# Kernel tuning notes

Measured on AMD Instinct MI355X. Metric: run time of the kernel, lower is better.

The kernel has to match this reference:

```python
import jax, jax.numpy as jnp
import numpy as np

B, S, D = 1, 4096, 2048
M = 4                  # compression rate
NC = S // M            # compressed slots
TOPK = 512
NH, C = 16, 64         # query heads, head dim
DC = 512               # query compression dim
NG, DG = 4, 512        # output projection groups, intermediate dim
CI, NHI = 64, 4        # indexer head dim, indexer heads
ROPE = 32              # partial rope dims (last ROPE of C)
EPS = 1e-6
NEG = -1e30


def _ln(x, w, b):
    mu = x.mean(-1, keepdims=True)
    var = ((x - mu) ** 2).mean(-1, keepdims=True)
    return (x - mu) * jax.lax.rsqrt(var + EPS) * w + b


def _rope(q, pos):
    # partial RoPE on the last ROPE dims of q [B,S,NH,C]; keys are NOT rotated (faithful)
    x_part, x_rope = q[..., :C - ROPE], q[..., C - ROPE:]
    x0, x1 = x_rope[..., 0::2], x_rope[..., 1::2]
    inv = 1.0 / (10000.0 ** (jnp.arange(0, ROPE, 2, dtype=jnp.float32) / ROPE))
    ang = pos[:, None].astype(jnp.float32) * inv[None]           # [S, ROPE/2]
    cos = jnp.cos(ang)[None, :, None, :]
    sin = jnp.sin(ang)[None, :, None, :]
    r = x0 * cos - x1 * sin
    i = x0 * sin + x1 * cos
    rot = jnp.stack([r, i], -1).reshape(x_rope.shape)
    return jnp.concatenate([x_part, rot], -1)


def reference(x, w_kv_a, w_kv_b, w_z_a, w_z_b, b_a, b_b, w_dq, w_iuq, w_w, w_k,
              w_uq, o_down, o_up, kvn_w, kvn_b, qn_w, qn_b, sink_logits):
    pos = jnp.arange(S)
    # ---- token-level compressor: windowed (2m-wide, m-stride) per-channel softmax ----
    c_a = (x @ w_kv_a).reshape(B, NC, M, C)
    c_b = (x @ w_kv_b).reshape(B, NC, M, C)
    z_a = (x @ w_z_a).reshape(B, NC, M, C)
    z_b = (x @ w_z_b).reshape(B, NC, M, C)
    prev_z = jnp.concatenate([jnp.full((B, 1, M, C), NEG, x.dtype), z_b[:, :-1]], 1)
    prev_c = jnp.concatenate([jnp.zeros((B, 1, M, C), x.dtype), c_b[:, :-1]], 1)
    logits = jnp.concatenate([prev_z + b_b, z_a + b_a], 2)        # [B,NC,2M,C]
    wts = jax.nn.softmax(logits, axis=2)
    compressed = (wts * jnp.concatenate([prev_c, c_a], 2)).sum(2)  # [B,NC,C]
    # ---- lightning indexer: relu multi-head scores + causal mask + top-k ----
    c_q = x @ w_dq                                                 # [B,S,DC]
    q_i = (c_q @ w_iuq).reshape(B, S, NHI, CI)
    hw = x @ w_w                                                   # [B,S,NHI]
    k_orig = x.reshape(B, NC, M, D).mean(2)
    k_proj = k_orig @ w_k                                          # [B,NC,CI]
    dot = jnp.einsum('bshc,bkc->bskh', q_i, k_proj)
    iscores = (jax.nn.relu(dot) * hw[:, :, None, :]).sum(-1)       # [B,S,NC]
    imask = jnp.arange(NC)[None, None, :] < pos[None, :, None]     # NC//S + 1 == 1
    iscores = jnp.where(imask, iscores, -jnp.inf)
    _, top_idx = jax.lax.top_k(iscores, TOPK)                      # [B,S,K]
    # ---- sparse attention over gathered compressed KV ----
    q = (c_q @ w_uq).reshape(B, S, NH, C)
    kc = _ln(compressed, kvn_w, kvn_b)
    q = _rope(_ln(q, qn_w, qn_b), pos)
    k_sel = kc[jnp.arange(B)[:, None, None], top_idx]              # [B,S,K,C]
    scores = jnp.einsum('bshc,bskc->bhsk', q, k_sel) / jnp.sqrt(jnp.float32(C))
    cmask = pos[None, None, :, None] < (top_idx[:, None, :, :] * M)
    scores = jnp.where(cmask, scores, -jnp.inf)
    e = jnp.exp(scores)
    denom = e.sum(-1, keepdims=True) + jnp.exp(sink_logits)[None, :, None, None]
    attn = e / denom                                               # sink-augmented softmax
    out = jnp.einsum('bhsk,bskc->bshc', attn, k_sel).reshape(B, S, NH * C)
    g = jnp.einsum('bsgd,gde->bsge', out.reshape(B, S, NG, (NH * C) // NG), o_down)
    return g.reshape(B, S, NG * DG) @ o_up


def setup_inputs() -> dict:
    key = jax.random.key(0)
    ks = jax.random.split(key, 20)
    lin = lambda k, fi, fo: jax.random.normal(k, (fi, fo), jnp.float32) / np.sqrt(fi)
    return {
        'x': jax.random.normal(ks[0], (B, S, D), jnp.float32),
        'w_kv_a': lin(ks[1], D, C), 'w_kv_b': lin(ks[2], D, C),
        'w_z_a': lin(ks[3], D, C), 'w_z_b': lin(ks[4], D, C),
        'b_a': 0.02 * jax.random.normal(ks[5], (M, C), jnp.float32),
        'b_b': 0.02 * jax.random.normal(ks[6], (M, C), jnp.float32),
        'w_dq': lin(ks[7], D, DC),
        'w_iuq': lin(ks[8], DC, CI * NHI),
        'w_w': lin(ks[9], D, NHI),
        'w_k': lin(ks[10], D, CI),
        'w_uq': lin(ks[11], DC, NH * C),
        'o_down': jax.random.normal(ks[12], (NG, (NH * C) // NG, DG), jnp.float32) / np.sqrt((NH * C) // NG),
        'o_up': lin(ks[13], NG * DG, D),
        'kvn_w': 1.0 + 0.02 * jax.random.normal(ks[14], (C,), jnp.float32),
        'kvn_b': 0.02 * jax.random.normal(ks[15], (C,), jnp.float32),
        'qn_w': 1.0 + 0.02 * jax.random.normal(ks[16], (C,), jnp.float32),
        'qn_b': 0.02 * jax.random.normal(ks[17], (C,), jnp.float32),
        'sink_logits': 0.02 * jax.random.normal(ks[18], (NH,), jnp.float32),
    }
```

## Files before the change

kernel.cpp:

```cpp
#include <hip/hip_runtime.h>
#include <math.h>

#define S_   4096
#define D_   2048
#define M_   4
#define NC_  1024
#define TOPK_ 512
#define NH_  16
#define C_   64
#define DC_  512
#define NG_  4
#define DG_  512
#define CI_  64
#define NHI_ 4
#define ROPE_ 32
#define EPS_ 1e-6f

typedef __attribute__((ext_vector_type(8))) short short8;
typedef __attribute__((ext_vector_type(4))) short short4v;
typedef __attribute__((ext_vector_type(4))) float floatx4;

__device__ inline unsigned short f2bf(float f) {
  unsigned u = __float_as_uint(f);
  u += 0x7fff + ((u >> 16) & 1);
  return (unsigned short)(u >> 16);
}
__device__ inline float bf2f(unsigned short h) {
  return __uint_as_float(((unsigned)h) << 16);
}

#define GLD16(src, dst) __builtin_amdgcn_global_load_lds( \
    (const __attribute__((address_space(1))) unsigned int*)(src), \
    (__attribute__((address_space(3))) unsigned int*)(dst), 16, 0, 0)

__device__ inline void xcd_remap(int& bx, int& by, int& bz) {
  int nx = gridDim.x, ny = gridDim.y;
  int flat = blockIdx.x + nx * (blockIdx.y + ny * blockIdx.z);
  int nwg = nx * ny * (int)gridDim.z;
  int swz = (flat & 7) * (nwg >> 3) + (flat >> 3);
  bx = swz % nx;
  int t = swz / nx;
  by = t % ny;
  bz = t / ny;
}

__global__ __launch_bounds__(256) void gemm_bf16_64(
    const unsigned short* __restrict__ A, const unsigned short* __restrict__ Bt,
    float* __restrict__ Cf, unsigned short* __restrict__ Cb,
    int K, int lda, int ldb, int ldc,
    long long Az, long long Bz, long long Cz) {
  int bx, by, zz;
  xcd_remap(bx, by, zz);
  A += (size_t)zz * Az;
  Bt += (size_t)zz * Bz;
  if (Cf) Cf += (size_t)zz * Cz;
  if (Cb) Cb += (size_t)zz * Cz;
  __shared__ unsigned short As[2 * 2 * 64 * 32];
  __shared__ unsigned short Bs[2 * 2 * 128 * 32];
  int tid = threadIdx.x;
  int bm = by * 64, bn = bx * 128;
  int lane = tid & 63, wid = tid >> 6;
  int wm = (wid & 1) * 32, wn = (wid >> 1) * 64;
  int qd = lane >> 4, m16 = lane & 15;

  floatx4 acc[2][4];
#pragma unroll
  for (int i = 0; i < 2; ++i)
#pragma unroll
    for (int j = 0; j < 4; ++j) acc[i][j] = (floatx4){0.f, 0.f, 0.f, 0.f};

  auto stage = [&](int buf, int kt) {
#pragma unroll
    for (int h = 0; h < 2; ++h) {
      {
        int rr = tid >> 2, ss = tid & 3;
        int gg = ss ^ ((rr >> 1) & 3);
        GLD16(A + (size_t)(bm + rr) * lda + kt + h * 32 + gg * 8,
              &As[(buf * 2 + h) * 2048 + tid * 8]);
      }
#pragma unroll
      for (int i = 0; i < 2; ++i) {
        int idx = tid + 256 * i;
        int rr = idx >> 2, ss = idx & 3;
        int gg = ss ^ ((rr >> 1) & 3);
        GLD16(Bt + (size_t)(bn + rr) * ldb + kt + h * 32 + gg * 8,
              &Bs[(buf * 2 + h) * 4096 + idx * 8]);
      }
    }
  };
  auto compute = [&](int buf) {
#pragma unroll
    for (int h = 0; h < 2; ++h) {
      const unsigned short* Ab = &As[(buf * 2 + h) * 2048];
      const unsigned short* Bb = &Bs[(buf * 2 + h) * 4096];
      short8 af[2], bfr[4];
#pragma unroll
      for (int mi = 0; mi < 2; ++mi) {
        int r = wm + mi * 16 + m16;
        int slot = qd ^ ((r >> 1) & 3);
        af[mi] = *(const short8*)&Ab[r * 32 + slot * 8];
      }
#pragma unroll
      for (int ni = 0; ni < 4; ++ni) {
        int r = wn + ni * 16 + m16;
        int slot = qd ^ ((r >> 1) & 3);
        bfr[ni] = *(const short8*)&Bb[r * 32 + slot * 8];
      }
#pragma unroll
      for (int mi = 0; mi < 2; ++mi)
#pragma unroll
        for (int ni = 0; ni < 4; ++ni)
          acc[mi][ni] = __builtin_amdgcn_mfma_f32_16x16x32_bf16(af[mi], bfr[ni], acc[mi][ni], 0, 0, 0);
    }
  };

  stage(0, 0);
  __syncthreads();
  int cur = 0;
  for (int kt = 64; kt < K; kt += 64) {
    stage(cur ^ 1, kt);
    compute(cur);
    __syncthreads();
    cur ^= 1;
  }
  compute(cur);

#pragma unroll
  for (int mi = 0; mi < 2; ++mi)
#pragma unroll
    for (int ni = 0; ni < 4; ++ni) {
      int col = bn + wn + ni * 16 + m16;
#pragma unroll
      for (int rg = 0; rg < 4; ++rg) {
        int row = bm + wm + mi * 16 + qd * 4 + rg;
        if (Cb)
          Cb[(size_t)row * ldc + col] = f2bf(acc[mi][ni][rg]);
        else
          Cf[(size_t)row * ldc + col] = acc[mi][ni][rg];
      }
    }
}

__global__ __launch_bounds__(256) void gemm_bf16_128(
    const unsigned short* __restrict__ A, const unsigned short* __restrict__ Bt,
    float* __restrict__ Cf, unsigned short* __restrict__ Cb,
    int K, int lda, int ldb, int ldc,
    long long Az, long long Bz, long long Cz) {
  int bx, by, zz;
  xcd_remap(bx, by, zz);
  A += (size_t)zz * Az;
  Bt += (size_t)zz * Bz;
  if (Cf) Cf += (size_t)zz * Cz;
  if (Cb) Cb += (size_t)zz * Cz;
  __shared__ unsigned short As[2 * 2 * 128 * 32];
  __shared__ unsigned short Bs[2 * 2 * 128 * 32];
  int tid = threadIdx.x;
  int bm = by * 128, bn = bx * 128;
  int lane = tid & 63, wid = tid >> 6;
  int wm = (wid & 1) * 64, wn = (wid >> 1) * 64;
  int qd = lane >> 4, m16 = lane & 15;

  floatx4 acc[4][4];
#pragma unroll
  for (int i = 0; i < 4; ++i)
#pragma unroll
    for (int j = 0; j < 4; ++j) acc[i][j] = (floatx4){0.f, 0.f, 0.f, 0.f};

  auto stage = [&](int buf, int kt) {
#pragma unroll
    for (int h = 0; h < 2; ++h) {
#pragma unroll
      for (int i = 0; i < 2; ++i) {
        int idx = tid + 256 * i;
        int rr = idx >> 2, ss = idx & 3;
        int gg = ss ^ ((rr >> 1) & 3);
        GLD16(A + (size_t)(bm + rr) * lda + kt + h * 32 + gg * 8,
              &As[(buf * 2 + h) * 4096 + idx * 8]);
        GLD16(Bt + (size_t)(bn + rr) * ldb + kt + h * 32 + gg * 8,
              &Bs[(buf * 2 + h) * 4096 + idx * 8]);
      }
    }
  };
  auto compute = [&](int buf) {
#pragma unroll
    for (int h = 0; h < 2; ++h) {
      const unsigned short* Ab = &As[(buf * 2 + h) * 4096];
      const unsigned short* Bb = &Bs[(buf * 2 + h) * 4096];
      short8 af[4], bfr[4];
#pragma unroll
      for (int mi = 0; mi < 4; ++mi) {
        int r = wm + mi * 16 + m16;
        int slot = qd ^ ((r >> 1) & 3);
        af[mi] = *(const short8*)&Ab[r * 32 + slot * 8];
      }
#pragma unroll
      for (int ni = 0; ni < 4; ++ni) {
        int r = wn + ni * 16 + m16;
        int slot = qd ^ ((r >> 1) & 3);
        bfr[ni] = *(const short8*)&Bb[r * 32 + slot * 8];
      }
#pragma unroll
      for (int mi = 0; mi < 4; ++mi)
#pragma unroll
        for (int ni = 0; ni < 4; ++ni)
          acc[mi][ni] = __builtin_amdgcn_mfma_f32_16x16x32_bf16(af[mi], bfr[ni], acc[mi][ni], 0, 0, 0);
    }
  };

  stage(0, 0);
  __syncthreads();
  int cur = 0;
  for (int kt = 64; kt < K; kt += 64) {
    stage(cur ^ 1, kt);
    compute(cur);
    __syncthreads();
    cur ^= 1;
  }
  compute(cur);

#pragma unroll
  for (int mi = 0; mi < 4; ++mi)
#pragma unroll
    for (int ni = 0; ni < 4; ++ni) {
      int col = bn + wn + ni * 16 + m16;
#pragma unroll
      for (int rg = 0; rg < 4; ++rg) {
        int row = bm + wm + mi * 16 + qd * 4 + rg;
        if (Cb)
          Cb[(size_t)row * ldc + col] = f2bf(acc[mi][ni][rg]);
        else
          Cf[(size_t)row * ldc + col] = acc[mi][ni][rg];
      }
    }
}

__global__ __launch_bounds__(256) void gemm_bf16_split_64(
    const unsigned short* __restrict__ Ah, const unsigned short* __restrict__ Al,
    const unsigned short* __restrict__ Bh, const unsigned short* __restrict__ Bl,
    float* __restrict__ Cf, int K, int lda, int ldb, int ldc,
    long long Az, long long Bz, long long Cz) {
  int bx, by, zz;
  xcd_remap(bx, by, zz);
  Ah += (size_t)zz * Az; Al += (size_t)zz * Az;
  Bh += (size_t)zz * Bz; Bl += (size_t)zz * Bz;
  Cf += (size_t)zz * Cz;
  __shared__ unsigned short Ash[64 * 32];
  __shared__ unsigned short Asl[64 * 32];
  __shared__ unsigned short Bsh[128 * 32];
  __shared__ unsigned short Bsl[128 * 32];
  int tid = threadIdx.x;
  int bm = by * 64, bn = bx * 128;
  int lane = tid & 63, wid = tid >> 6;
  int wm = (wid & 1) * 32, wn = (wid >> 1) * 64;
  int qd = lane >> 4, m16 = lane & 15;

  floatx4 acc[2][4];
#pragma unroll
  for (int i = 0; i < 2; ++i)
#pragma unroll
    for (int j = 0; j < 4; ++j) acc[i][j] = (floatx4){0.f, 0.f, 0.f, 0.f};

  for (int k0 = 0; k0 < K; k0 += 32) {
    {
      int r = tid >> 2, sl = tid & 3;
      int g = sl ^ ((r >> 1) & 3);
      size_t aoff = (size_t)(bm + r) * lda + k0 + g * 8;
      GLD16(Ah + aoff, &Ash[tid * 8]);
      GLD16(Al + aoff, &Asl[tid * 8]);
    }
#pragma unroll
    for (int i = 0; i < 2; ++i) {
      int idx = tid + 256 * i;
      int r = idx >> 2, sl = idx & 3;
      int g = sl ^ ((r >> 1) & 3);
      size_t boff = (size_t)(bn + r) * ldb + k0 + g * 8;
      GLD16(Bh + boff, &Bsh[idx * 8]);
      GLD16(Bl + boff, &Bsl[idx * 8]);
    }
    __syncthreads();
    short8 afh[2], afl[2], bfh[4], bfl[4];
#pragma unroll
    for (int mi = 0; mi < 2; ++mi) {
      int r = wm + mi * 16 + m16;
      int slot = qd ^ ((r >> 1) & 3);
      afh[mi] = *(const short8*)&Ash[r * 32 + slot * 8];
      afl[mi] = *(const short8*)&Asl[r * 32 + slot * 8];
    }
#pragma unroll
    for (int ni = 0; ni < 4; ++ni) {
      int r = wn + ni * 16 + m16;
      int slot = qd ^ ((r >> 1) & 3);
      bfh[ni] = *(const short8*)&Bsh[r * 32 + slot * 8];
      bfl[ni] = *(const short8*)&Bsl[r * 32 + slot * 8];
    }
#pragma unroll
    for (int mi = 0; mi < 2; ++mi)
#pragma unroll
      for (int ni = 0; ni < 4; ++ni) {
        acc[mi][ni] = __builtin_amdgcn_mfma_f32_16x16x32_bf16(afh[mi], bfh[ni], acc[mi][ni], 0, 0, 0);
        acc[mi][ni] = __builtin_amdgcn_mfma_f32_16x16x32_bf16(afh[mi], bfl[ni], acc[mi][ni], 0, 0, 0);
        acc[mi][ni] = __builtin_amdgcn_mfma_f32_16x16x32_bf16(afl[mi], bfh[ni], acc[mi][ni], 0, 0, 0);
      }
    __syncthreads();
  }
#pragma unroll
  for (int mi = 0; mi < 2; ++mi)
#pragma unroll
    for (int ni = 0; ni < 4; ++ni) {
      int col = bn + wn + ni * 16 + m16;
#pragma unroll
      for (int rg = 0; rg < 4; ++rg) {
        int row = bm + wm + mi * 16 + qd * 4 + rg;
        Cf[(size_t)row * ldc + col] = acc[mi][ni][rg];
      }
    }
}

__global__ __launch_bounds__(256) void gemm_bf16_split_128(
    const unsigned short* __restrict__ Ah, const unsigned short* __restrict__ Al,
    const unsigned short* __restrict__ Bh, const unsigned short* __restrict__ Bl,
    float* __restrict__ Cf, int K, int lda, int ldb, int ldc,
    long long Az, long long Bz, long long Cz) {
  int bx, by, zz;
  xcd_remap(bx, by, zz);
  Ah += (size_t)zz * Az; Al += (size_t)zz * Az;
  Bh += (size_t)zz * Bz; Bl += (size_t)zz * Bz;
  Cf += (size_t)zz * Cz;
  __shared__ unsigned short Ash[2 * 128 * 32];
  __shared__ unsigned short Asl[2 * 128 * 32];
  __shared__ unsigned short Bsh[2 * 128 * 32];
  __shared__ unsigned short Bsl[2 * 128 * 32];
  int tid = threadIdx.x;
  int bm = by * 128, bn = bx * 128;
  int lane = tid & 63, wid = tid >> 6;
  int wm = (wid & 1) * 64, wn = (wid >> 1) * 64;
  int qd = lane >> 4, m16 = lane & 15;

  floatx4 acc[4][4];
#pragma unroll
  for (int i = 0; i < 4; ++i)
#pragma unroll
    for (int j = 0; j < 4; ++j) acc[i][j] = (floatx4){0.f, 0.f, 0.f, 0.f};

  auto stage = [&](int buf, int kt) {
#pragma unroll
    for (int i = 0; i < 2; ++i) {
      int idx = tid + 256 * i;
      int rr = idx >> 2, ss = idx & 3;
      int gg = ss ^ ((rr >> 1) & 3);
      size_t aoff = (size_t)(bm + rr) * lda + kt + gg * 8;
      size_t boff = (size_t)(bn + rr) * ldb + kt + gg * 8;
      GLD16(Ah + aoff, &Ash[buf * 4096 + idx * 8]);
      GLD16(Al + aoff, &Asl[buf * 4096 + idx * 8]);
      GLD16(Bh + boff, &Bsh[buf * 4096 + idx * 8]);
      GLD16(Bl + boff, &Bsl[buf * 4096 + idx * 8]);
    }
  };
  auto compute = [&](int buf) {
    const unsigned short* Ahb = &Ash[buf * 4096];
    const unsigned short* Alb = &Asl[buf * 4096];
    const unsigned short* Bhb = &Bsh[buf * 4096];
    const unsigned short* Blb = &Bsl[buf * 4096];
    short8 afh[4], afl[4], bfh[4], bfl[4];
#pragma unroll
    for (int mi = 0; mi < 4; ++mi) {
      int r = wm + mi * 16 + m16;
      int slot = qd ^ ((r >> 1) & 3);
      afh[mi] = *(const short8*)&Ahb[r * 32 + slot * 8];
      afl[mi] = *(const short8*)&Alb[r * 32 + slot * 8];
    }
#pragma unroll
    for (int ni = 0; ni < 4; ++ni) {
      int r = wn + ni * 16 + m16;
      int slot = qd ^ ((r >> 1) & 3);
      bfh[ni] = *(const short8*)&Bhb[r * 32 + slot * 8];
      bfl[ni] = *(const short8*)&Blb[r * 32 + slot * 8];
    }
#pragma unroll
    for (int mi = 0; mi < 4; ++mi)
#pragma unroll
      for (int ni = 0; ni < 4; ++ni) {
        acc[mi][ni] = __builtin_amdgcn_mfma_f32_16x16x32_bf16(afh[mi], bfh[ni], acc[mi][ni], 0, 0, 0);
        acc[mi][ni] = __builtin_amdgcn_mfma_f32_16x16x32_bf16(afh[mi], bfl[ni], acc[mi][ni], 0, 0, 0);
        acc[mi][ni] = __builtin_amdgcn_mfma_f32_16x16x32_bf16(afl[mi], bfh[ni], acc[mi][ni], 0, 0, 0);
      }
  };

  stage(0, 0);
  __syncthreads();
  int cur = 0;
  for (int kt = 32; kt < K; kt += 32) {
    stage(cur ^ 1, kt);
    compute(cur);
    __syncthreads();
    cur ^= 1;
  }
  compute(cur);

#pragma unroll
  for (int mi = 0; mi < 4; ++mi)
#pragma unroll
    for (int ni = 0; ni < 4; ++ni) {
      int col = bn + wn + ni * 16 + m16;
#pragma unroll
      for (int rg = 0; rg < 4; ++rg) {
        int row = bm + wm + mi * 16 + qd * 4 + rg;
        Cf[(size_t)row * ldc + col] = acc[mi][ni][rg];
      }
    }
}

__global__ void reduce_f32(const float* __restrict__ P, float* __restrict__ C, int n, int z) {
  int i = (blockIdx.x * 256 + threadIdx.x) * 4;
  if (i >= n) return;
  float4 a = *(const float4*)&P[i];
  for (int s = 1; s < z; ++s) {
    float4 b = *(const float4*)&P[(size_t)s * n + i];
    a.x += b.x; a.y += b.y; a.z += b.z; a.w += b.w;
  }
  *(float4*)&C[i] = a;
}

__global__ void reduce_cast_split(const float* __restrict__ P, unsigned short* __restrict__ hi,
                                  unsigned short* __restrict__ lo, int n, int z) {
  int i = (blockIdx.x * 256 + threadIdx.x) * 4;
  if (i >= n) return;
  float4 a = *(const float4*)&P[i];
  for (int s = 1; s < z; ++s) {
    float4 b = *(const float4*)&P[(size_t)s * n + i];
    a.x += b.x; a.y += b.y; a.z += b.z; a.w += b.w;
  }
  ushort4 h = make_ushort4(f2bf(a.x), f2bf(a.y), f2bf(a.z), f2bf(a.w));
  ushort4 l = make_ushort4(f2bf(a.x - bf2f(h.x)), f2bf(a.y - bf2f(h.y)),
                           f2bf(a.z - bf2f(h.z)), f2bf(a.w - bf2f(h.w)));
  *(ushort4*)&hi[i] = h;
  *(ushort4*)&lo[i] = l;
}

__global__ __launch_bounds__(256) void iscores_mfma(
    const unsigned short* __restrict__ Ah, const unsigned short* __restrict__ Al,
    const unsigned short* __restrict__ Bh, const unsigned short* __restrict__ Bl,
    const float* __restrict__ hw, float* __restrict__ isc) {
  int bm = blockIdx.y * 128, bn = blockIdx.x * 128;
  if (bn > (bm >> 2) + 30) return;
  __shared__ unsigned short Ash[128 * 32];
  __shared__ unsigned short Asl[128 * 32];
  __shared__ unsigned short Bsh[128 * 32];
  __shared__ unsigned short Bsl[128 * 32];
  int tid = threadIdx.x;
  int lane = tid & 63, wid = tid >> 6;
  int wm = (wid >> 1) * 64, wn = (wid & 1) * 64;
  int qd = lane >> 4, m16 = lane & 15;

  floatx4 acc[4][4];
#pragma unroll
  for (int i = 0; i < 4; ++i)
#pragma unroll
    for (int j = 0; j < 4; ++j) acc[i][j] = (floatx4){0.f, 0.f, 0.f, 0.f};

#pragma unroll
  for (int k0 = 0; k0 < 64; k0 += 32) {
#pragma unroll
    for (int i = 0; i < 2; ++i) {
      int idx = tid + 256 * i;
      int r = idx >> 2, s = idx & 3;
      int g = s ^ ((r >> 1) & 3);
      size_t aoff = (size_t)(bm + r) * 64 + k0 + g * 8;
      size_t boff = (size_t)(bn + r) * 64 + k0 + g * 8;
      GLD16(Ah + aoff, &Ash[idx * 8]);
      GLD16(Al + aoff, &Asl[idx * 8]);
      GLD16(Bh + boff, &Bsh[idx * 8]);
      GLD16(Bl + boff, &Bsl[idx * 8]);
    }
    __syncthreads();
    short8 afh[4], afl[4], bfh[4], bfl[4];
#pragma unroll
    for (int mi = 0; mi < 4; ++mi) {
      int r = wm + mi * 16 + m16;
      int slot = qd ^ ((r >> 1) & 3);
      afh[mi] = *(const short8*)&Ash[r * 32 + slot * 8];
      afl[mi] = *(const short8*)&Asl[r * 32 + slot * 8];
    }
#pragma unroll
    for (int ni = 0; ni < 4; ++ni) {
      int r = wn + ni * 16 + m16;
      int slot = qd ^ ((r >> 1) & 3);
      bfh[ni] = *(const short8*)&Bsh[r * 32 + slot * 8];
      bfl[ni] = *(const short8*)&Bsl[r * 32 + slot * 8];
    }
#pragma unroll
    for (int mi = 0; mi < 4; ++mi)
#pragma unroll
      for (int ni = 0; ni < 4; ++ni) {
        acc[mi][ni] = __builtin_amdgcn_mfma_f32_16x16x32_bf16(afh[mi], bfh[ni], acc[mi][ni], 0, 0, 0);
        acc[mi][ni] = __builtin_amdgcn_mfma_f32_16x16x32_bf16(afh[mi], bfl[ni], acc[mi][ni], 0, 0, 0);
        acc[mi][ni] = __builtin_amdgcn_mfma_f32_16x16x32_bf16(afl[mi], bfh[ni], acc[mi][ni], 0, 0, 0);
      }
    __syncthreads();
  }
#pragma unroll
  for (int mi = 0; mi < 4; ++mi) {
    int tok = ((bm + wm + mi * 16) >> 2) + qd;
    float4 hwv = *(const float4*)&hw[tok * 4];
#pragma unroll
    for (int ni = 0; ni < 4; ++ni) {
      floatx4 a = acc[mi][ni];
      float v = fmaxf(a[0], 0.f) * hwv.x + fmaxf(a[1], 0.f) * hwv.y +
                fmaxf(a[2], 0.f) * hwv.z + fmaxf(a[3], 0.f) * hwv.w;
      int col = bn + wn + ni * 16 + m16;
      isc[(size_t)tok * NC_ + col] = (col < tok) ? v : -__builtin_inff();
    }
  }
}

#define BM 64
#define BN 64
#define BK 16
#define KSL_ 16
#define KSLICE_ 128
__global__ __launch_bounds__(256) void gemm_f32_splitk(
    const float* __restrict__ A, const float* __restrict__ B,
    float* __restrict__ P, int lda, int ldb) {
  __shared__ float As[BK][BM + 4];
  __shared__ float Bs[BK][BN + 4];
  int tid = threadIdx.x;
  int bm = blockIdx.y * BM;
  int kbase = blockIdx.x * KSLICE_;
  int tr = tid >> 4;
  int tc = tid & 15;
  float acc[4][4] = {{0.f}};
  for (int k0 = kbase; k0 < kbase + KSLICE_; k0 += BK) {
    int ac = tid & 15;
    int ar0 = tid >> 4;
#pragma unroll
    for (int i = 0; i < 4; ++i) {
      int r = ar0 + 16 * i;
      As[ac][r] = A[(size_t)(bm + r) * lda + k0 + ac];
    }
    int bc = tid & 63;
    int br0 = tid >> 6;
#pragma unroll
    for (int i = 0; i < 4; ++i) {
      int r = br0 + 4 * i;
      Bs[r][bc] = B[(size_t)(k0 + r) * ldb + bc];
    }
    __syncthreads();
#pragma unroll
    for (int kk = 0; kk < BK; ++kk) {
      float4 av = *(const float4*)&As[kk][tr * 4];
      float4 bv = *(const float4*)&Bs[kk][tc * 4];
      float a[4] = {av.x, av.y, av.z, av.w};
      float b[4] = {bv.x, bv.y, bv.z, bv.w};
#pragma unroll
      for (int i = 0; i < 4; ++i)
#pragma unroll
        for (int j = 0; j < 4; ++j) acc[i][j] += a[i] * b[j];
    }
    __syncthreads();
  }
  float* Pb = P + (size_t)blockIdx.x * (NC_ * CI_);
#pragma unroll
  for (int i = 0; i < 4; ++i) {
    float4 v = make_float4(acc[i][0], acc[i][1], acc[i][2], acc[i][3]);
    *(float4*)&Pb[(size_t)(bm + tr * 4 + i) * CI_ + tc * 4] = v;
  }
}

__global__ void reduce_splitk_cast(const float* __restrict__ P,
                                   unsigned short* __restrict__ hi,
                                   unsigned short* __restrict__ lo) {
  int i = blockIdx.x * 256 + threadIdx.x;
  float a = 0.f;
#pragma unroll
  for (int s = 0; s < KSL_; ++s) a += P[(size_t)s * (NC_ * CI_) + i];
  unsigned short h = f2bf(a);
  hi[i] = h;
  lo[i] = f2bf(a - bf2f(h));
}

__device__ inline float wave_sum64(float v) {
#pragma unroll
  for (int off = 32; off > 0; off >>= 1) v += __shfl_xor(v, off, 64);
  return v;
}

__global__ __launch_bounds__(512) void cast_split_hw_mean(
    const float* __restrict__ x, unsigned short* __restrict__ hi,
    unsigned short* __restrict__ lo, const float* __restrict__ ww,
    float* __restrict__ hw, float* __restrict__ ko) {
  int j = blockIdx.x, tid = threadIdx.x;
  int d0 = tid * 4;
  const float* wr = ww + d0 * 4;
  float4 v[4];
  float a[4][4];
#pragma unroll
  for (int m = 0; m < 4; ++m) {
    size_t i = (size_t)(j * 4 + m) * D_ + d0;
    v[m] = *(const float4*)&x[i];
    ushort4 h = make_ushort4(f2bf(v[m].x), f2bf(v[m].y), f2bf(v[m].z), f2bf(v[m].w));
    ushort4 l = make_ushort4(f2bf(v[m].x - bf2f(h.x)), f2bf(v[m].y - bf2f(h.y)),
                             f2bf(v[m].z - bf2f(h.z)), f2bf(v[m].w - bf2f(h.w)));
    *(ushort4*)&hi[i] = h;
    *(ushort4*)&lo[i] = l;
    a[m][0] = v[m].x * wr[0] + v[m].y * wr[4] + v[m].z * wr[8]  + v[m].w * wr[12];
    a[m][1] = v[m].x * wr[1] + v[m].y * wr[5] + v[m].z * wr[9]  + v[m].w * wr[13];
    a[m][2] = v[m].x * wr[2] + v[m].y * wr[6] + v[m].z * wr[10] + v[m].w * wr[14];
    a[m][3] = v[m].x * wr[3] + v[m].y * wr[7] + v[m].z * wr[11] + v[m].w * wr[15];
  }
  float4 s4;
  s4.x = 0.25f * (v[0].x + v[1].x + v[2].x + v[3].x);
  s4.y = 0.25f * (v[0].y + v[1].y + v[2].y + v[3].y);
  s4.z = 0.25f * (v[0].z + v[1].z + v[2].z + v[3].z);
  s4.w = 0.25f * (v[0].w + v[1].w + v[2].w + v[3].w);
  *(float4*)&ko[(size_t)j * D_ + d0] = s4;
#pragma unroll
  for (int m = 0; m < 4; ++m)
#pragma unroll
    for (int h2 = 0; h2 < 4; ++h2) a[m][h2] = wave_sum64(a[m][h2]);
  __shared__ float red[8][16];
  int wid = tid >> 6, lane = tid & 63;
  if (lane == 0) {
#pragma unroll
    for (int m = 0; m < 4; ++m)
#pragma unroll
      for (int h2 = 0; h2 < 4; ++h2) red[wid][m * 4 + h2] = a[m][h2];
  }
  __syncthreads();
  if (tid < 16) {
    float acc = 0.f;
#pragma unroll
    for (int w2 = 0; w2 < 8; ++w2) acc += red[w2][tid];
    hw[(size_t)(j * 4 + (tid >> 2)) * 4 + (tid & 3)] = acc;
  }
}

__global__ __launch_bounds__(256) void prep_kernel(
    const float* __restrict__ w_kv_a, const float* __restrict__ w_kv_b,
    const float* __restrict__ w_z_a, const float* __restrict__ w_z_b,
    unsigned short* __restrict__ wpackT,
    const float* __restrict__ w_dq, unsigned short* __restrict__ wdqTh,
    unsigned short* __restrict__ wdqTl,
    const float* __restrict__ w_iuq, unsigned short* __restrict__ wiuqTh,
    unsigned short* __restrict__ wiuqTl,
    const float* __restrict__ w_uq, unsigned short* __restrict__ wuqT,
    const float* __restrict__ o_down, unsigned short* __restrict__ odb,
    const float* __restrict__ o_up, unsigned short* __restrict__ oupT,
    float* __restrict__ rt) {
  __shared__ float t[32][33];
  int b = blockIdx.x;
  int tid = threadIdx.x;
  int tx = tid & 31, ty = tid >> 5;
  if (b < 512) {
    int wsel = b >> 7, local = b & 127;
    int bx = local & 63, by = local >> 6;
    const float* in = (wsel == 0) ? w_kv_a : (wsel == 1) ? w_kv_b : (wsel == 2) ? w_z_a : w_z_b;
    unsigned short* outp = wpackT + wsel * 64 * 2048;
    int k0 = bx * 32, n0 = by * 32;
#pragma unroll
    for (int i = 0; i < 4; ++i)
      t[ty * 4 + i][tx] = in[(size_t)(k0 + ty * 4 + i) * 64 + n0 + tx];
    __syncthreads();
#pragma unroll
    for (int i = 0; i < 4; ++i)
      outp[(size_t)(n0 + ty * 4 + i) * 2048 + k0 + tx] = f2bf(t[tx][ty * 4 + i]);
  } else if (b < 1536) {
    int local = b - 512;
    int bx = local & 63, by = local >> 6;
    int k0 = bx * 32, n0 = by * 32;
#pragma unroll
    for (int i = 0; i < 4; ++i)
      t[ty * 4 + i][tx] = w_dq[(size_t)(k0 + ty * 4 + i) * 512 + n0 + tx];
    __syncthreads();
#pragma unroll
    for (int i = 0; i < 4; ++i) {
      float v = t[tx][ty * 4 + i];
      unsigned short h = f2bf(v);
      wdqTh[(size_t)(n0 + ty * 4 + i) * 2048 + k0 + tx] = h;
      wdqTl[(size_t)(n0 + ty * 4 + i) * 2048 + k0 + tx] = f2bf(v - bf2f(h));
    }
  } else if (b < 1664) {
    int local = b - 1536;
    int bx = local & 15, by = local >> 4;
    int k0 = bx * 32, n0 = by * 32;
#pragma unroll
    for (int i = 0; i < 4; ++i)
      t[ty * 4 + i][tx] = w_iuq[(size_t)(k0 + ty * 4 + i) * 256 + n0 + tx];
    __syncthreads();
#pragma unroll
    for (int i = 0; i < 4; ++i) {
      float v = t[tx][ty * 4 + i];
      unsigned short h = f2bf(v);
      wiuqTh[(size_t)(n0 + ty * 4 + i) * 512 + k0 + tx] = h;
      wiuqTl[(size_t)(n0 + ty * 4 + i) * 512 + k0 + tx] = f2bf(v - bf2f(h));
    }
  } else if (b < 2176) {
    int local = b - 1664;
    int bx = local & 15, by = local >> 4;
    int k0 = bx * 32, n0 = by * 32;
#pragma unroll
    for (int i = 0; i < 4; ++i)
      t[ty * 4 + i][tx] = w_uq[(size_t)(k0 + ty * 4 + i) * 1024 + n0 + tx];
    __syncthreads();
#pragma unroll
    for (int i = 0; i < 4; ++i)
      wuqT[(size_t)(n0 + ty * 4 + i) * 512 + k0 + tx] = f2bf(t[tx][ty * 4 + i]);
  } else if (b < 2688) {
    int i = ((b - 2176) * 256 + tid) * 4;
    float4 v = *(const float4*)&o_down[i];
    ushort4 o = make_ushort4(f2bf(v.x), f2bf(v.y), f2bf(v.z), f2bf(v.w));
    *(ushort4*)&odb[i] = o;
  } else if (b < 6784) {
    int local = b - 2688;
    int bx = local & 63, by = local >> 6;
    int k0 = bx * 32, n0 = by * 32;
#pragma unroll
    for (int i = 0; i < 4; ++i)
      t[ty * 4 + i][tx] = o_up[(size_t)(k0 + ty * 4 + i) * 2048 + n0 + tx];
    __syncthreads();
#pragma unroll
    for (int i = 0; i < 4; ++i)
      oupT[(size_t)(n0 + ty * 4 + i) * 2048 + k0 + tx] = f2bf(t[tx][ty * 4 + i]);
  } else {
    int i = (b - 6784) * 256 + tid;
    int s = i >> 4, p = i & 15;
    float inv = powf(10000.f, -(2.f * (float)p) / (float)ROPE_);
    float ang = (float)s * inv;
    rt[i * 2] = cosf(ang);
    rt[i * 2 + 1] = sinf(ang);
  }
}

__global__ void gate_ln_kernel(const float* __restrict__ c4,
                               const float* __restrict__ ba, const float* __restrict__ bb,
                               const float* __restrict__ w, const float* __restrict__ bias,
                               unsigned short* __restrict__ kcb,
                               unsigned short* __restrict__ kcbT) {
  int i = blockIdx.x * 256 + threadIdx.x;
  int j = i >> 6, c = i & 63;
  float lg[8], vv[8];
#pragma unroll
  for (int m = 0; m < 4; ++m) {
    if (j == 0) {
      lg[m] = -1e30f + bb[m * C_ + c];
      vv[m] = 0.f;
    } else {
      int row = (j - 1) * 4 + m;
      lg[m] = c4[(size_t)row * 256 + 192 + c] + bb[m * C_ + c];
      vv[m] = c4[(size_t)row * 256 + 64 + c];
    }
    int row2 = j * 4 + m;
    lg[4 + m] = c4[(size_t)row2 * 256 + 128 + c] + ba[m * C_ + c];
    vv[4 + m] = c4[(size_t)row2 * 256 + 0 + c];
  }
  float mx = lg[0];
#pragma unroll
  for (int t = 1; t < 8; ++t) mx = fmaxf(mx, lg[t]);
  float se = 0.f, acc = 0.f;
#pragma unroll
  for (int t = 0; t < 8; ++t) {
    float e = expf(lg[t] - mx);
    se += e;
    acc += e * vv[t];
  }
  float cv = acc / se;
  float mu = wave_sum64(cv) * (1.f / 64.f);
  float d = cv - mu;
  float var = wave_sum64(d * d) * (1.f / 64.f);
  float y = d * (1.f / sqrtf(var + EPS_)) * w[c] + bias[c];
  unsigned short h = f2bf(y);
  kcb[(size_t)j * C_ + c] = h;
  kcbT[(size_t)c * NC_ + j] = h;
}

__global__ void ln_rope_q_kernel(const float* __restrict__ quq, const float* __restrict__ w,
                                 const float* __restrict__ b, const float* __restrict__ rt,
                                 unsigned short* __restrict__ qb) {
  int row = blockIdx.x * 4 + (threadIdx.x >> 6);
  int s = row >> 4;
  int c = threadIdx.x & 63;
  float v = quq[(size_t)row * C_ + c];
  float mu = wave_sum64(v) * (1.f / 64.f);
  float d = v - mu;
  float var = wave_sum64(d * d) * (1.f / 64.f);
  float y = d * (1.f / sqrtf(var + EPS_)) * w[c] + b[c];
  float outv;
  float partner = __shfl_xor(y, 1, 64);
  if (c < C_ - ROPE_) {
    outv = y;
  } else {
    int p = (c - (C_ - ROPE_)) >> 1;
    float cs = rt[(s * 16 + p) * 2];
    float sn = rt[(s * 16 + p) * 2 + 1];
    if ((c & 1) == 0)
      outv = y * cs - partner * sn;
    else
      outv = partner * sn + y * cs;
  }
  qb[(size_t)row * C_ + c] = f2bf(outv * 0.125f);
}

#define MINF_ 0x007FFFFFu
__global__ __launch_bounds__(256) void topk_select_kernel(
    const float* __restrict__ isc, unsigned* __restrict__ sel) {
  __shared__ unsigned mv[NC_];
  __shared__ unsigned bins[256];
  __shared__ unsigned wsum[4];
  __shared__ unsigned sB, sR;
  __shared__ unsigned selw[32];
  int s = blockIdx.x;
  int tid = threadIdx.x;
  int w = tid >> 6, lane = tid & 63;
  if (tid < 32) selw[tid] = 0u;
  for (int i = tid; i < NC_; i += 256) {
    if (i < s) {
      unsigned u = __float_as_uint(isc[(size_t)s * NC_ + i]);
      mv[i] = (u & 0x80000000u) ? ~u : (u | 0x80000000u);
    } else {
      mv[i] = MINF_;
    }
  }
  __syncthreads();
  unsigned K_rem = TOPK_;
  unsigned prefix = 0u;
  for (int lvl = 0; lvl < 4; ++lvl) {
    int shift = 24 - 8 * lvl;
    unsigned pm = (lvl == 0) ? 0u : (0xFFFFFFFFu << (32 - 8 * lvl));
    bins[tid] = 0u;
    __syncthreads();
    for (int i = tid; i < NC_; i += 256) {
      unsigned m = mv[i];
      if ((m & pm) == prefix) atomicAdd(&bins[(m >> shift) & 0xFFu], 1u);
    }
    __syncthreads();
    unsigned v = bins[tid];
    unsigned p = v;
#pragma unroll
    for (int off = 1; off < 64; off <<= 1) {
      unsigned n = __shfl_up(p, (unsigned)off, 64);
      if (lane >= off) p += n;
    }
    if (lane == 63) wsum[w] = p;
    __syncthreads();
    unsigned T = 0, woff = 0;
#pragma unroll
    for (int i = 0; i < 4; ++i) {
      unsigned x_ = wsum[i];
      T += x_;
      if (i < w) woff += x_;
    }
    p += woff;
    unsigned gt = T - p;
    if (gt < K_rem && K_rem <= gt + v) { sB = (unsigned)tid; sR = K_rem - gt; }
    __syncthreads();
    prefix |= (sB << shift);
    K_rem = sR;
  }
  unsigned vstar = prefix;
  unsigned eq = 0;
#pragma unroll
  for (int j = 0; j < 4; ++j) eq += (mv[4 * tid + j] == vstar);
  unsigned rp = eq;
#pragma unroll
  for (int off = 1; off < 64; off <<= 1) {
    unsigned n = __shfl_up(rp, (unsigned)off, 64);
    if (lane >= off) rp += n;
  }
  if (lane == 63) wsum[w] = rp;
  __syncthreads();
  unsigned woff2 = 0;
#pragma unroll
  for (int i = 0; i < 4; ++i)
    if (i < w) woff2 += wsum[i];
  unsigned rank0 = rp + woff2 - eq;
  unsigned local = 0, bits = 0;
#pragma unroll
  for (int j = 0; j < 4; ++j) {
    unsigned m = mv[4 * tid + j];
    int idx = 4 * tid + j;
    bool sb = ((m > vstar) || (m == vstar && (rank0 + local) < K_rem)) && (s < 4 * idx);
    local += (m == vstar);
    if (sb) bits |= (1u << (idx & 31));
  }
  if (bits) atomicOr(&selw[tid >> 3], bits);
  __syncthreads();
  if (tid < 32) sel[(size_t)s * 32 + tid] = selw[tid];
}

#define TS_ 8
__global__ __launch_bounds__(256) void attn_mfma_kernel(
    const unsigned short* __restrict__ qb, const unsigned short* __restrict__ kcb,
    const unsigned short* __restrict__ kcbT, const unsigned* __restrict__ sel,
    const float* __restrict__ sink, unsigned short* __restrict__ out) {
  __shared__ unsigned short p_s[128 * 68];
  __shared__ unsigned selw[TS_][32];
  int tid = threadIdx.x;
  int s0 = blockIdx.x * TS_;
  int lane = tid & 63, w = tid >> 6;
  int qd = lane >> 4, m16 = lane & 15;

  selw[tid >> 5][tid & 31] = sel[(size_t)(s0 + (tid >> 5)) * 32 + (tid & 31)];

  short8 qf[2][2];
#pragma unroll
  for (int tk = 0; tk < 2; ++tk)
#pragma unroll
    for (int ks = 0; ks < 2; ++ks)
      qf[tk][ks] = *(const short8*)&qb[(size_t)(s0 + 2 * w + tk) * 1024 + m16 * 64 + ks * 32 + qd * 8];

  floatx4 of[2][4];
#pragma unroll
  for (int i = 0; i < 2; ++i)
#pragma unroll
    for (int j = 0; j < 4; ++j) of[i][j] = (floatx4){0.f, 0.f, 0.f, 0.f};
  float dsum[2] = {0.f, 0.f};

  int ub = max(511, s0 + TS_ - 2);
  int ct_start = max(0, (s0 + 4) >> 8);
  int ct_end = min(16, (ub >> 6) + 1);

  for (int ct = ct_start; ct < ct_end; ++ct) {
    int c0 = ct * 64;
#pragma unroll
    for (int mc = 0; mc < 4; ++mc) {
      short8 a0 = *(const short8*)&kcb[(size_t)(c0 + mc * 16 + m16) * 64 + qd * 8];
      short8 a1 = *(const short8*)&kcb[(size_t)(c0 + mc * 16 + m16) * 64 + 32 + qd * 8];
#pragma unroll
      for (int nt = 0; nt < 2; ++nt) {
        floatx4 sc = (floatx4){0.f, 0.f, 0.f, 0.f};
        sc = __builtin_amdgcn_mfma_f32_16x16x32_bf16(a0, qf[nt][0], sc, 0, 0, 0);
        sc = __builtin_amdgcn_mfma_f32_16x16x32_bf16(a1, qf[nt][1], sc, 0, 0, 0);
        int tokL = 2 * w + nt;
        unsigned sw = selw[tokL][ct * 2 + (mc >> 1)];
        short4v pv;
#pragma unroll
        for (int rg = 0; rg < 4; ++rg) {
          int bitpos = (mc * 16 + qd * 4 + rg) & 31;
          bool ok = ((sw >> bitpos) & 1u) != 0u;
          float e = ok ? __expf(sc[rg]) : 0.f;
          dsum[nt] += e;
          pv[rg] = (short)f2bf(e);
        }
        *(short4v*)&p_s[(tokL * 16 + m16) * 68 + mc * 16 + qd * 4] = pv;
      }
    }
#pragma unroll
    for (int ks = 0; ks < 2; ++ks) {
      short8 pa0 = *(const short8*)&p_s[((2 * w + 0) * 16 + m16) * 68 + ks * 32 + qd * 8];
      short8 pa1 = *(const short8*)&p_s[((2 * w + 1) * 16 + m16) * 68 + ks * 32 + qd * 8];
#pragma unroll
      for (int nt = 0; nt < 4; ++nt) {
        short8 bv = *(const short8*)&kcbT[(size_t)(nt * 16 + m16) * NC_ + c0 + ks * 32 + qd * 8];
        of[0][nt] = __builtin_amdgcn_mfma_f32_16x16x32_bf16(pa0, bv, of[0][nt], 0, 0, 0);
        of[1][nt] = __builtin_amdgcn_mfma_f32_16x16x32_bf16(pa1, bv, of[1][nt], 0, 0, 0);
      }
    }
  }
#pragma unroll
  for (int nt = 0; nt < 2; ++nt) {
    dsum[nt] += __shfl_xor(dsum[nt], 16, 64);
    dsum[nt] += __shfl_xor(dsum[nt], 32, 64);
  }
#pragma unroll
  for (int tk = 0; tk < 2; ++tk)
#pragma unroll
    for (int nt = 0; nt < 4; ++nt) {
      floatx4 o = of[tk][nt];
#pragma unroll
      for (int rg = 0; rg < 4; ++rg) {
        int head = qd * 4 + rg;
        float dn = __shfl(dsum[tk], head, 64) + __expf(sink[head]);
        out[(size_t)(s0 + 2 * w + tk) * 1024 + head * 64 + nt * 16 + m16] = f2bf(o[rg] / dn);
      }
    }
}

#define OFF_QUQ    0u
#define OFF_Q      4194304u
#define OFF_XH     8388608u
#define OFF_XL     12582912u
#define OFF_PART   16777216u
#define OFF_KO     18874368u
#define OFF_C4     20971520u
#define OFF_CQF    22020096u
#define OFF_RT     23134208u
#define OFF_WTB    24117248u
#define OFF_CQH    25165824u
#define OFF_CQL    26214400u
#define OFF_WPACKT 27262976u
#define OFF_WDQTH  27525120u
#define OFF_WDQTL  28049408u
#define OFF_WIUQTH 28573696u
#define OFF_WIUQTL 28639232u
#define OFF_WUQT   28704768u
#define OFF_ODB    28966912u
#define OFF_OUPT   29229056u
#define OFF_HW     31326208u
#define OFF_KC     31408128u
#define OFF_KPR    31473664u

extern "C" void kernel_launch(void* const* d_in, const int* in_sizes, int n_in,
                              void* d_out, int out_size, void* d_ws, size_t ws_size,
                              hipStream_t stream) {
  const float* x      = (const float*)d_in[0];
  const float* w_kv_a = (const float*)d_in[1];
  const float* w_kv_b = (const float*)d_in[2];
  const float* w_z_a  = (const float*)d_in[3];
  const float* w_z_b  = (const float*)d_in[4];
  const float* b_a    = (const float*)d_in[5];
  const float* b_b    = (const float*)d_in[6];
  const float* w_dq   = (const float*)d_in[7];
  const float* w_iuq  = (const float*)d_in[8];
  const float* w_w    = (const float*)d_in[9];
  const float* w_k    = (const float*)d_in[10];
  const float* w_uq   = (const float*)d_in[11];
  const float* o_down = (const float*)d_in[12];
  const float* o_up   = (const float*)d_in[13];
  const float* kvn_w  = (const float*)d_in[14];
  const float* kvn_b  = (const float*)d_in[15];
  const float* qn_w   = (const float*)d_in[16];
  const float* qn_b   = (const float*)d_in[17];
  const float* sink   = (const float*)d_in[18];
  float* out = (float*)d_out;
  float* ws = (float*)d_ws;

  float* quq   = ws + OFF_QUQ;
  float* isc   = ws + OFF_QUQ;
  unsigned short* qb = (unsigned short*)(ws + OFF_Q);
  unsigned short* xh = (unsigned short*)(ws + OFF_XH);
  unsigned short* xl = (unsigned short*)(ws + OFF_XL);
  unsigned* sel = (unsigned*)(ws + OFF_XL);
  float* part  = ws + OFF_PART;
  float* k_or  = ws + OFF_KO;
  unsigned short* attnb = (unsigned short*)(ws + OFF_KO);
  float* c4    = ws + OFF_C4;
  unsigned short* qih = (unsigned short*)(ws + OFF_CQF);
  unsigned short* qil = qih + S_ * NHI_ * CI_;
  unsigned short* kph = qil + S_ * NHI_ * CI_;
  unsigned short* kpl = kph + NC_ * CI_;
  float* rt    = ws + OFF_RT;
  unsigned short* wtb = (unsigned short*)(ws + OFF_WTB);
  unsigned short* cqh = (unsigned short*)(ws + OFF_CQH);
  unsigned short* cql = (unsigned short*)(ws + OFF_CQL);
  unsigned short* wpackT = (unsigned short*)(ws + OFF_WPACKT);
  unsigned short* wdqTh  = (unsigned short*)(ws + OFF_WDQTH);
  unsigned short* wdqTl  = (unsigned short*)(ws + OFF_WDQTL);
  unsigned short* wiuqTh = (unsigned short*)(ws + OFF_WIUQTH);
  unsigned short* wiuqTl = (unsigned short*)(ws + OFF_WIUQTL);
  unsigned short* wuqT   = (unsigned short*)(ws + OFF_WUQT);
  unsigned short* odb    = (unsigned short*)(ws + OFF_ODB);
  unsigned short* oupT   = (unsigned short*)(ws + OFF_OUPT);
  float* hw    = ws + OFF_HW;
  unsigned short* kcb  = (unsigned short*)(ws + OFF_KC);
  unsigned short* kcbT = kcb + NC_ * C_;

  dim3 blk(256);

  cast_split_hw_mean<<<NC_, dim3(512), 0, stream>>>(x, xh, xl, w_w, hw, k_or);
  prep_kernel<<<7040, blk, 0, stream>>>(w_kv_a, w_kv_b, w_z_a, w_z_b, wpackT,
                                        w_dq, wdqTh, wdqTl, w_iuq, wiuqTh, wiuqTl,
                                        w_uq, wuqT, o_down, odb, o_up, oupT, rt);

  gemm_bf16_64<<<dim3(2, 32, 4), blk, 0, stream>>>(
      oupT, odb, nullptr, wtb, DG_, D_, DG_, NG_ * 256,
      (long long)DG_, (long long)256 * DG_, 256LL);

  gemm_f32_splitk<<<dim3(KSL_, 16), blk, 0, stream>>>(k_or, w_k, part, D_, CI_);
  reduce_splitk_cast<<<256, blk, 0, stream>>>(part, kph, kpl);

  gemm_bf16_split_128<<<dim3(4, 32, 4), blk, 0, stream>>>(xh, xl, wdqTh, wdqTl, ws,
                                                          512, D_, D_, DC_, 512, 512, (long long)S_ * DC_);
  reduce_cast_split<<<2048, blk, 0, stream>>>(ws, cqh, cql, S_ * DC_, 4);
  gemm_bf16_64<<<dim3(2, 64, 4), blk, 0, stream>>>(xh, wpackT, part, nullptr,
                                                   512, D_, D_, 256, 512, 512, (long long)S_ * 256);
  reduce_f32<<<1024, blk, 0, stream>>>(part, c4, S_ * 256, 4);
  gemm_bf16_split_64<<<dim3(2, 64, 4), blk, 0, stream>>>(cqh, cql, wiuqTh, wiuqTl, part,
                                                         128, DC_, DC_, 256, 128, 128, (long long)S_ * 256);
  reduce_cast_split<<<1024, blk, 0, stream>>>(part, qih, qil, S_ * 256, 4);
  gemm_bf16_64<<<dim3(8, 64, 1), blk, 0, stream>>>(cqh, wuqT, quq, nullptr,
                                                   DC_, DC_, DC_, NH_ * C_, 0, 0, 0);

  gate_ln_kernel<<<256, blk, 0, stream>>>(c4, b_a, b_b, kvn_w, kvn_b, kcb, kcbT);

  ln_rope_q_kernel<<<16384, blk, 0, stream>>>(quq, qn_w, qn_b, rt, qb);

  iscores_mfma<<<dim3(8, 128), blk, 0, stream>>>(qih, qil, kph, kpl, hw, isc);
  topk_select_kernel<<<S_, blk, 0, stream>>>(isc, sel);

  attn_mfma_kernel<<<S_ / TS_, blk, 0, stream>>>(qb, kcb, kcbT, sel, sink, attnb);

  gemm_bf16_128<<<dim3(16, 32, 1), blk, 0, stream>>>(attnb, wtb, out, nullptr,
                                                     NG_ * 256, NH_ * C_, NG_ * 256, D_, 0, 0, 0);
}
```

Measured before the change: 390.5 us.

## Split attention over key tiles into two slices with a combine kernel

New measurement: 391.6 us. Within noise of the previous version (+0.3%).

```diff
diff --git a/kernel.cpp b/kernel.cpp
--- a/kernel.cpp
+++ b/kernel.cpp
@@ -887,14 +887,16 @@
 }
 
 #define TS_ 8
-__global__ __launch_bounds__(256) void attn_mfma_kernel(
+#define OFSL_ 8388608u
+__global__ __launch_bounds__(256) void attn_mfma_split(
     const unsigned short* __restrict__ qb, const unsigned short* __restrict__ kcb,
     const unsigned short* __restrict__ kcbT, const unsigned* __restrict__ sel,
-    const float* __restrict__ sink, unsigned short* __restrict__ out) {
+    float* __restrict__ ofp, float* __restrict__ dsp) {
   __shared__ unsigned short p_s[128 * 68];
   __shared__ unsigned selw[TS_][32];
   int tid = threadIdx.x;
   int s0 = blockIdx.x * TS_;
+  int slice = blockIdx.y;
   int lane = tid & 63, w = tid >> 6;
   int qd = lane >> 4, m16 = lane & 15;
 
@@ -915,10 +917,13 @@
   float dsum[2] = {0.f, 0.f};
 
   int ub = max(511, s0 + TS_ - 2);
-  int ct_start = max(0, (s0 + 4) >> 8);
-  int ct_end = min(16, (ub >> 6) + 1);
-
-  for (int ct = ct_start; ct < ct_end; ++ct) {
+  int cs = max(0, (s0 + 4) >> 8);
+  int ce = min(16, (ub >> 6) + 1);
+  int mid = (cs + ce + 1) >> 1;
+  int t0 = slice ? mid : cs;
+  int t1 = slice ? ce : mid;
+
+  for (int ct = t0; ct < t1; ++ct) {
     int c0 = ct * 64;
 #pragma unroll
     for (int mc = 0; mc < 4; ++mc) {
@@ -960,6 +965,11 @@
     dsum[nt] += __shfl_xor(dsum[nt], 16, 64);
     dsum[nt] += __shfl_xor(dsum[nt], 32, 64);
   }
+  if (lane < 16) {
+#pragma unroll
+    for (int tk = 0; tk < 2; ++tk)
+      dsp[(size_t)slice * S_ * 16 + (size_t)(s0 + 2 * w + tk) * 16 + lane] = dsum[tk];
+  }
 #pragma unroll
   for (int tk = 0; tk < 2; ++tk)
 #pragma unroll
@@ -968,10 +978,24 @@
 #pragma unroll
       for (int rg = 0; rg < 4; ++rg) {
         int head = qd * 4 + rg;
-        float dn = __shfl(dsum[tk], head, 64) + __expf(sink[head]);
-        out[(size_t)(s0 + 2 * w + tk) * 1024 + head * 64 + nt * 16 + m16] = f2bf(o[rg] / dn);
-      }
-    }
+        ofp[(size_t)slice * OFSL_ + (size_t)(s0 + 2 * w + tk) * 1024 + head * 64 + nt * 16 + m16] = o[rg];
+      }
+    }
+}
+
+__global__ void attn_combine(const float* __restrict__ ofp, const float* __restrict__ dsp,
+                             const float* __restrict__ sink, unsigned short* __restrict__ out) {
+  int i = (blockIdx.x * 256 + threadIdx.x) * 4;
+  int tok = i >> 10;
+  int head = (i & 1023) >> 6;
+  float4 a = *(const float4*)&ofp[i];
+  float4 b = *(const float4*)&ofp[(size_t)OFSL_ + i];
+  float dn = dsp[(size_t)tok * 16 + head] + dsp[(size_t)S_ * 16 + (size_t)tok * 16 + head] +
+             __expf(sink[head]);
+  float inv = 1.f / dn;
+  ushort4 o = make_ushort4(f2bf((a.x + b.x) * inv), f2bf((a.y + b.y) * inv),
+                           f2bf((a.z + b.z) * inv), f2bf((a.w + b.w) * inv));
+  *(ushort4*)&out[i] = o;
 }
 
 #define OFF_QUQ    0u
@@ -1025,11 +1049,13 @@
 
   float* quq   = ws + OFF_QUQ;
   float* isc   = ws + OFF_QUQ;
+  float* ofp   = ws + OFF_QUQ;
   unsigned short* qb = (unsigned short*)(ws + OFF_Q);
   unsigned short* xh = (unsigned short*)(ws + OFF_XH);
   unsigned short* xl = (unsigned short*)(ws + OFF_XL);
   unsigned* sel = (unsigned*)(ws + OFF_XL);
   float* part  = ws + OFF_PART;
+  float* dsp   = ws + OFF_PART;
   float* k_or  = ws + OFF_KO;
   unsigned short* attnb = (unsigned short*)(ws + OFF_KO);
   float* c4    = ws + OFF_C4;
@@ -1086,7 +1112,8 @@
   iscores_mfma<<<dim3(8, 128), blk, 0, stream>>>(qih, qil, kph, kpl, hw, isc);
   topk_select_kernel<<<S_, blk, 0, stream>>>(isc, sel);
 
-  attn_mfma_kernel<<<S_ / TS_, blk, 0, stream>>>(qb, kcb, kcbT, sel, sink, attnb);
+  attn_mfma_split<<<dim3(S_ / TS_, 2), blk, 0, stream>>>(qb, kcb, kcbT, sel, ofp, dsp);
+  attn_combine<<<S_ * 1024 / 4 / 256, blk, 0, stream>>>(ofp, dsp, sink, attnb);
 
   gemm_bf16_128<<<dim3(16, 32, 1), blk, 0, stream>>>(attnb, wtb, out, nullptr,
                                                      NG_ * 256, NH_ * C_, NG_ * 256, D_, 0, 0, 0);
```

## Fuse split-K reduction into gate_ln and shrink attention blocks to one wave

Applied to the files above, without the earlier changes.

Measured after the change: 384.6 us, median of 2. No clear change (-1.5%).

```diff
diff --git a/kernel.cpp b/kernel.cpp
--- a/kernel.cpp
+++ b/kernel.cpp
@@ -408,17 +408,6 @@
         Cf[(size_t)row * ldc + col] = acc[mi][ni][rg];
       }
     }
-}
-
-__global__ void reduce_f32(const float* __restrict__ P, float* __restrict__ C, int n, int z) {
-  int i = (blockIdx.x * 256 + threadIdx.x) * 4;
-  if (i >= n) return;
-  float4 a = *(const float4*)&P[i];
-  for (int s = 1; s < z; ++s) {
-    float4 b = *(const float4*)&P[(size_t)s * n + i];
-    a.x += b.x; a.y += b.y; a.z += b.z; a.w += b.w;
-  }
-  *(float4*)&C[i] = a;
 }
 
 __global__ void reduce_cast_split(const float* __restrict__ P, unsigned short* __restrict__ hi,
@@ -730,11 +719,12 @@
   }
 }
 
-__global__ void gate_ln_kernel(const float* __restrict__ c4,
+__global__ void gate_ln_kernel(const float* __restrict__ P,
                                const float* __restrict__ ba, const float* __restrict__ bb,
                                const float* __restrict__ w, const float* __restrict__ bias,
                                unsigned short* __restrict__ kcb,
                                unsigned short* __restrict__ kcbT) {
+  const size_t n = (size_t)S_ * 256;
   int i = blockIdx.x * 256 + threadIdx.x;
   int j = i >> 6, c = i & 63;
   float lg[8], vv[8];
@@ -744,13 +734,21 @@
       lg[m] = -1e30f + bb[m * C_ + c];
       vv[m] = 0.f;
     } else {
-      int row = (j - 1) * 4 + m;
-      lg[m] = c4[(size_t)row * 256 + 192 + c] + bb[m * C_ + c];
-      vv[m] = c4[(size_t)row * 256 + 64 + c];
-    }
-    int row2 = j * 4 + m;
-    lg[4 + m] = c4[(size_t)row2 * 256 + 128 + c] + ba[m * C_ + c];
-    vv[4 + m] = c4[(size_t)row2 * 256 + 0 + c];
+      size_t idxz = (size_t)((j - 1) * 4 + m) * 256 + 192 + c;
+      size_t idxc = (size_t)((j - 1) * 4 + m) * 256 + 64 + c;
+      float az = P[idxz], ac = P[idxc];
+#pragma unroll
+      for (int s = 1; s < 4; ++s) { az += P[s * n + idxz]; ac += P[s * n + idxc]; }
+      lg[m] = az + bb[m * C_ + c];
+      vv[m] = ac;
+    }
+    size_t idxz2 = (size_t)(j * 4 + m) * 256 + 128 + c;
+    size_t idxc2 = (size_t)(j * 4 + m) * 256 + 0 + c;
+    float az2 = P[idxz2], ac2 = P[idxc2];
+#pragma unroll
+    for (int s = 1; s < 4; ++s) { az2 += P[s * n + idxz2]; ac2 += P[s * n + idxc2]; }
+    lg[4 + m] = az2 + ba[m * C_ + c];
+    vv[4 + m] = ac2;
   }
   float mx = lg[0];
 #pragma unroll
@@ -886,16 +884,16 @@
   if (tid < 32) sel[(size_t)s * 32 + tid] = selw[tid];
 }
 
-#define TS_ 8
-__global__ __launch_bounds__(256) void attn_mfma_kernel(
+#define TS_ 2
+__global__ __launch_bounds__(64) void attn_mfma_kernel(
     const unsigned short* __restrict__ qb, const unsigned short* __restrict__ kcb,
     const unsigned short* __restrict__ kcbT, const unsigned* __restrict__ sel,
     const float* __restrict__ sink, unsigned short* __restrict__ out) {
-  __shared__ unsigned short p_s[128 * 68];
+  __shared__ unsigned short p_s[32 * 68];
   __shared__ unsigned selw[TS_][32];
   int tid = threadIdx.x;
   int s0 = blockIdx.x * TS_;
-  int lane = tid & 63, w = tid >> 6;
+  int lane = tid & 63;
   int qd = lane >> 4, m16 = lane & 15;
 
   selw[tid >> 5][tid & 31] = sel[(size_t)(s0 + (tid >> 5)) * 32 + (tid & 31)];
@@ -905,7 +903,7 @@
   for (int tk = 0; tk < 2; ++tk)
 #pragma unroll
     for (int ks = 0; ks < 2; ++ks)
-      qf[tk][ks] = *(const short8*)&qb[(size_t)(s0 + 2 * w + tk) * 1024 + m16 * 64 + ks * 32 + qd * 8];
+      qf[tk][ks] = *(const short8*)&qb[(size_t)(s0 + tk) * 1024 + m16 * 64 + ks * 32 + qd * 8];
 
   floatx4 of[2][4];
 #pragma unroll
@@ -915,10 +913,10 @@
   float dsum[2] = {0.f, 0.f};
 
   int ub = max(511, s0 + TS_ - 2);
-  int ct_start = max(0, (s0 + 4) >> 8);
-  int ct_end = min(16, (ub >> 6) + 1);
-
-  for (int ct = ct_start; ct < ct_end; ++ct) {
+  int cs = max(0, (s0 + 4) >> 8);
+  int ce = min(16, (ub >> 6) + 1);
+
+  for (int ct = cs; ct < ce; ++ct) {
     int c0 = ct * 64;
 #pragma unroll
     for (int mc = 0; mc < 4; ++mc) {
@@ -929,8 +927,7 @@
         floatx4 sc = (floatx4){0.f, 0.f, 0.f, 0.f};
         sc = __builtin_amdgcn_mfma_f32_16x16x32_bf16(a0, qf[nt][0], sc, 0, 0, 0);
         sc = __builtin_amdgcn_mfma_f32_16x16x32_bf16(a1, qf[nt][1], sc, 0, 0, 0);
-        int tokL = 2 * w + nt;
-        unsigned sw = selw[tokL][ct * 2 + (mc >> 1)];
+        unsigned sw = selw[nt][ct * 2 + (mc >> 1)];
         short4v pv;
 #pragma unroll
         for (int rg = 0; rg < 4; ++rg) {
@@ -940,13 +937,13 @@
           dsum[nt] += e;
           pv[rg] = (short)f2bf(e);
         }
-        *(short4v*)&p_s[(tokL * 16 + m16) * 68 + mc * 16 + qd * 4] = pv;
+        *(short4v*)&p_s[(nt * 16 + m16) * 68 + mc * 16 + qd * 4] = pv;
       }
     }
 #pragma unroll
     for (int ks = 0; ks < 2; ++ks) {
-      short8 pa0 = *(const short8*)&p_s[((2 * w + 0) * 16 + m16) * 68 + ks * 32 + qd * 8];
-      short8 pa1 = *(const short8*)&p_s[((2 * w + 1) * 16 + m16) * 68 + ks * 32 + qd * 8];
+      short8 pa0 = *(const short8*)&p_s[(0 * 16 + m16) * 68 + ks * 32 + qd * 8];
+      short8 pa1 = *(const short8*)&p_s[(1 * 16 + m16) * 68 + ks * 32 + qd * 8];
 #pragma unroll
       for (int nt = 0; nt < 4; ++nt) {
         short8 bv = *(const short8*)&kcbT[(size_t)(nt * 16 + m16) * NC_ + c0 + ks * 32 + qd * 8];
@@ -969,7 +966,7 @@
       for (int rg = 0; rg < 4; ++rg) {
         int head = qd * 4 + rg;
         float dn = __shfl(dsum[tk], head, 64) + __expf(sink[head]);
-        out[(size_t)(s0 + 2 * w + tk) * 1024 + head * 64 + nt * 16 + m16] = f2bf(o[rg] / dn);
+        out[(size_t)(s0 + tk) * 1024 + head * 64 + nt * 16 + m16] = f2bf(o[rg] / dn);
       }
     }
 }
@@ -980,7 +977,6 @@
 #define OFF_XL     12582912u
 #define OFF_PART   16777216u
 #define OFF_KO     18874368u
-#define OFF_C4     20971520u
 #define OFF_CQF    22020096u
 #define OFF_RT     23134208u
 #define OFF_WTB    24117248u
@@ -1032,7 +1028,6 @@
   float* part  = ws + OFF_PART;
   float* k_or  = ws + OFF_KO;
   unsigned short* attnb = (unsigned short*)(ws + OFF_KO);
-  float* c4    = ws + OFF_C4;
   unsigned short* qih = (unsigned short*)(ws + OFF_CQF);
   unsigned short* qil = qih + S_ * NHI_ * CI_;
   unsigned short* kph = qil + S_ * NHI_ * CI_;
@@ -1072,21 +1067,19 @@
   reduce_cast_split<<<2048, blk, 0, stream>>>(ws, cqh, cql, S_ * DC_, 4);
   gemm_bf16_64<<<dim3(2, 64, 4), blk, 0, stream>>>(xh, wpackT, part, nullptr,
                                                    512, D_, D_, 256, 512, 512, (long long)S_ * 256);
-  reduce_f32<<<1024, blk, 0, stream>>>(part, c4, S_ * 256, 4);
+  gate_ln_kernel<<<256, blk, 0, stream>>>(part, b_a, b_b, kvn_w, kvn_b, kcb, kcbT);
   gemm_bf16_split_64<<<dim3(2, 64, 4), blk, 0, stream>>>(cqh, cql, wiuqTh, wiuqTl, part,
                                                          128, DC_, DC_, 256, 128, 128, (long long)S_ * 256);
   reduce_cast_split<<<1024, blk, 0, stream>>>(part, qih, qil, S_ * 256, 4);
   gemm_bf16_64<<<dim3(8, 64, 1), blk, 0, stream>>>(cqh, wuqT, quq, nullptr,
                                                    DC_, DC_, DC_, NH_ * C_, 0, 0, 0);
 
-  gate_ln_kernel<<<256, blk, 0, stream>>>(c4, b_a, b_b, kvn_w, kvn_b, kcb, kcbT);
-
   ln_rope_q_kernel<<<16384, blk, 0, stream>>>(quq, qn_w, qn_b, rt, qb);
 
   iscores_mfma<<<dim3(8, 128), blk, 0, stream>>>(qih, qil, kph, kpl, hw, isc);
   topk_select_kernel<<<S_, blk, 0, stream>>>(isc, sel);
 
-  attn_mfma_kernel<<<S_ / TS_, blk, 0, stream>>>(qb, kcb, kcbT, sel, sink, attnb);
+  attn_mfma_kernel<<<S_ / TS_, dim3(64), 0, stream>>>(qb, kcb, kcbT, sel, sink, attnb);
 
   gemm_bf16_128<<<dim3(16, 32, 1), blk, 0, stream>>>(attnb, wtb, out, nullptr,
                                                      NG_ * 256, NH_ * C_, NG_ * 256, D_, 0, 0, 0);
```
